# Kernel optimization log

Measured on AMD Instinct MI355X. Metric: run time of the kernel, lower is better.

The kernel has to match this reference:

```python
import jax, jax.numpy as jnp
import numpy as np

EPS = 1e-12  # F.normalize eps
G = 8        # groups (init g)
NC = 32      # num_cluster
LMD = 2


def _l2norm(v, axis):
    n = jnp.sqrt(jnp.sum(v * v, axis=axis, keepdims=True))
    return v / jnp.maximum(n, EPS)


def setup_inputs() -> dict:
    key = jax.random.key(0)
    ks = jax.random.split(key, 6)
    b, m, d = 32, 512, 1024
    d2 = LMD * d                 # 2048
    nd = d2 // G                 # 256 = new_dims
    x = jax.random.normal(ks[0], (b, m, d), dtype=jnp.float32)
    mask = jnp.ones((b, m), dtype=bool)
    # Linear params with torch-like fan-in scaling
    We = jax.random.normal(ks[1], (d2, d), dtype=jnp.float32) / np.sqrt(d)
    be = jnp.zeros((d2,), dtype=jnp.float32)
    W1 = jax.random.normal(ks[2], (G * NC, d2), dtype=jnp.float32) / np.sqrt(d2)
    b1 = jnp.zeros((G * NC,), dtype=jnp.float32)
    W2 = jax.random.normal(ks[3], (G, d2), dtype=jnp.float32) / np.sqrt(d2)
    b2 = jnp.zeros((G,), dtype=jnp.float32)
    centroid = jax.random.uniform(ks[4], (NC, nd), dtype=jnp.float32)
    return {"x": x, "mask": mask, "We": We, "be": be, "W1": W1, "b1": b1,
            "W2": W2, "b2": b2, "centroid": centroid}


def reference(x, mask, We, be, W1, b1, W2, b2, centroid):
    b, m, d = x.shape
    # BaseAggregator: L2 normalize along feature dim (mask unused)
    xn = _l2norm(x, axis=2)
    xe = jnp.einsum('bmd,ed->bme', xn, We) + be          # (b, m, lmd*d)
    a1 = jax.nn.softmax((jnp.einsum('bme,ke->bmk', xe, W1) + b1)
                        .reshape(b, m, G, NC), axis=3)   # (b, m, G, nc)
    a2 = jax.nn.softmax(jnp.einsum('bme,ge->bmg', xe, W2) + b2, axis=2)  # (b, m, G)
    xg = xe.reshape(b, m, G, -1)                         # (b, m, G, new_dims)
    # sum_nc a1*(x - c) = x*sum(a1) - a1@c = x - a1@c  (softmax sums to 1)
    cent = jnp.einsum('bmgk,kd->bmgd', a1, centroid)     # (b, m, G, new_dims)
    v = jnp.einsum('bmg,bmgd->bd', a2, xg - cent) / m    # sum over G, mean over m
    return _l2norm(v, axis=1)
```

## Files before the change

### kernel.cpp

```cpp
#include <hip/hip_runtime.h>
#include <hip/hip_bf16.h>
#include <stdint.h>

#define B_BATCH 32
#define M_SEQ   512
#define R_TOT   16384
#define D_IN    1024
#define E_DIM   2048
#define NCAT    384
#define NVALID  264

typedef float  f32x4 __attribute__((ext_vector_type(4)));
typedef short  s16x8 __attribute__((ext_vector_type(8)));

__device__ __forceinline__ uint16_t f2bf(float f) {
  uint32_t u = __builtin_bit_cast(uint32_t, f);
  uint32_t r = (u + 0x7fffu + ((u >> 16) & 1u)) >> 16;
  return (uint16_t)r;
}
__device__ __forceinline__ float bf2f(uint16_t u) {
  return __builtin_bit_cast(float, (uint32_t)u << 16);
}

__device__ __forceinline__ f32x4 mfma_bf16(s16x8 a, s16x8 b, f32x4 c) {
  return __builtin_amdgcn_mfma_f32_16x16x32_bf16(a, b, c, 0, 0, 0);
}

typedef __attribute__((address_space(3))) void lds_void_t;
typedef const __attribute__((address_space(1))) void gbl_void_t;
__device__ __forceinline__ void async_load16(const void* g, void* l) {
  __builtin_amdgcn_global_load_lds((gbl_void_t*)g, (lds_void_t*)l, 16, 0, 0);
}

#define FENCE() __builtin_amdgcn_sched_barrier(0)
#define PH_PRE_NL() do { FENCE(); __builtin_amdgcn_s_barrier(); FENCE(); \
                         __builtin_amdgcn_s_setprio(1); } while (0)
#define PH_POST() do { __builtin_amdgcn_s_setprio(0); FENCE(); \
                       __builtin_amdgcn_s_barrier(); FENCE(); } while (0)

__global__ void zero_buf(float* __restrict__ p, int n) {
  int i = blockIdx.x * blockDim.x + threadIdx.x;
  if (i < n) p[i] = 0.0f;
}

__global__ void cvt_bf16(const float* __restrict__ src, uint16_t* __restrict__ dst, int n) {
  int i = blockIdx.x * blockDim.x + threadIdx.x;
  if (i < n) dst[i] = f2bf(src[i]);
}

__global__ void build_wcat(const float* __restrict__ W1, const float* __restrict__ W2,
                           uint16_t* __restrict__ wcat) {
  int i = blockIdx.x * blockDim.x + threadIdx.x;
  if (i >= NCAT * E_DIM) return;
  int row = i >> 11, col = i & (E_DIM - 1);
  float v = 0.0f;
  if (row < 256) v = W1[i];
  else if (row < NVALID) v = W2[(row - 256) * E_DIM + col];
  wcat[i] = f2bf(v);
}

__global__ void build_bcat(const float* __restrict__ b1, const float* __restrict__ b2,
                           float* __restrict__ bcat) {
  int i = blockIdx.x * blockDim.x + threadIdx.x;
  if (i >= NCAT) return;
  float v = 0.0f;
  if (i < 256) v = b1[i];
  else if (i < NVALID) v = b2[i - 256];
  bcat[i] = v;
}

__global__ __launch_bounds__(256) void normalize_rows(const float* __restrict__ x,
                                                      uint16_t* __restrict__ xn) {
  const int r = blockIdx.x, tid = threadIdx.x;
  const float4* xr = (const float4*)(x + (size_t)r * D_IN);
  float4 v = xr[tid];
  float ss = v.x * v.x + v.y * v.y + v.z * v.z + v.w * v.w;
  #pragma unroll
  for (int m = 32; m; m >>= 1) ss += __shfl_xor(ss, m);
  __shared__ float wsum[4];
  if ((tid & 63) == 0) wsum[tid >> 6] = ss;
  __syncthreads();
  float tot = wsum[0] + wsum[1] + wsum[2] + wsum[3];
  float scale = 1.0f / fmaxf(sqrtf(tot), 1e-12f);
  uint16_t* o = xn + (size_t)r * D_IN + tid * 4;
  o[0] = f2bf(v.x * scale); o[1] = f2bf(v.y * scale);
  o[2] = f2bf(v.z * scale); o[3] = f2bf(v.w * scale);
}

template <int KDIM>
__global__ __launch_bounds__(512, 2) void gemm256(
    const uint16_t* __restrict__ A, const uint16_t* __restrict__ B,
    const float* __restrict__ bias, uint16_t* __restrict__ C, int N) {
  __shared__ uint16_t lds[65536];
  constexpr int NT = KDIM / 64;
  const int tid = threadIdx.x;
  const int w = tid >> 6, lane = tid & 63;
  const int wr = w >> 2, wc = w & 3;
  const int bm = blockIdx.x, bn = blockIdx.y;

  const int srow = tid >> 3;
  const int scol = (((tid & 7) ^ (srow & 7)) << 3);
  const int l15 = lane & 15, l4 = lane >> 4, lx = lane & 7;
  const int ck0 = ((l4) ^ lx) << 4;
  const int ck1 = ((4 + l4) ^ lx) << 4;

  const int arow0 = bm * 256, brow0 = bn * 256;

  auto STAGE = [&](const uint16_t* __restrict__ M, int grow0, int tile,
                   int bufi, int mat, int half) {
    if (tile >= NT) return;
    const uint16_t* src = M + (size_t)(grow0 + half * 128 + srow) * KDIM + tile * 64 + scol;
    uint16_t* dst = lds + ((bufi * 2 + mat) * 2 + half) * 8192 + w * 512;
    async_load16(src, dst);
    async_load16(src + (size_t)64 * KDIM, dst + 4096);
  };
  auto LDA = [&](int bufi, int mi, int ckb) -> s16x8 {
    return *(const s16x8*)((const char*)(lds + ((bufi * 2 + 0) * 2 + wr) * 8192)
                           + (mi * 16 + l15) * 128 + ckb);
  };
  auto LDB = [&](int bufi, int ni, int ckb) -> s16x8 {
    return *(const s16x8*)((const char*)(lds + ((bufi * 2 + 1) * 2 + (wc >> 1)) * 8192)
                           + ((wc & 1) * 64 + ni * 16 + l15) * 128 + ckb);
  };

  f32x4 acc[8][4] = {};
  s16x8 aLo[4][2], aHi[4][2], bLo[2][2], bHi[2][2];

  auto R1 = [&](int buf) {
    #pragma unroll
    for (int mi = 0; mi < 4; ++mi) { aLo[mi][0] = LDA(buf, mi, ck0); aLo[mi][1] = LDA(buf, mi, ck1); }
    #pragma unroll
    for (int ni = 0; ni < 2; ++ni) { bLo[ni][0] = LDB(buf, ni, ck0); bLo[ni][1] = LDB(buf, ni, ck1); }
  };
  auto R2 = [&](int buf) {
    #pragma unroll
    for (int j = 0; j < 2; ++j) { bHi[j][0] = LDB(buf, 2 + j, ck0); bHi[j][1] = LDB(buf, 2 + j, ck1); }
  };
  auto R3 = [&](int buf) {
    #pragma unroll
    for (int mi = 0; mi < 4; ++mi) { aHi[mi][0] = LDA(buf, 4 + mi, ck0); aHi[mi][1] = LDA(buf, 4 + mi, ck1); }
  };

  auto MM1 = [&] {
    #pragma unroll
    for (int kk = 0; kk < 2; ++kk)
      #pragma unroll
      for (int mi = 0; mi < 4; ++mi)
        #pragma unroll
        for (int ni = 0; ni < 2; ++ni)
          acc[mi][ni] = mfma_bf16(aLo[mi][kk], bLo[ni][kk], acc[mi][ni]);
  };
  auto MM2 = [&] {
    #pragma unroll
    for (int kk = 0; kk < 2; ++kk)
      #pragma unroll
      for (int mi = 0; mi < 4; ++mi)
        #pragma unroll
        for (int j = 0; j < 2; ++j)
          acc[mi][2 + j] = mfma_bf16(aLo[mi][kk], bHi[j][kk], acc[mi][2 + j]);
  };
  auto MM3 = [&] {
    #pragma unroll
    for (int kk = 0; kk < 2; ++kk)
      #pragma unroll
      for (int mi = 0; mi < 4; ++mi)
        #pragma unroll
        for (int ni = 0; ni < 2; ++ni)
          acc[4 + mi][ni] = mfma_bf16(aHi[mi][kk], bLo[ni][kk], acc[4 + mi][ni]);
  };
  auto MM4 = [&] {
    #pragma unroll
    for (int kk = 0; kk < 2; ++kk)
      #pragma unroll
      for (int mi = 0; mi < 4; ++mi)
        #pragma unroll
        for (int j = 0; j < 2; ++j)
          acc[4 + mi][2 + j] = mfma_bf16(aHi[mi][kk], bHi[j][kk], acc[4 + mi][2 + j]);
  };

#define GROUP(H, T, VM0, FINAL) do {                                           \
    STAGE(A, arow0, (T) + 1, (H) ^ 1, 0, 0);                                   \
    PH_PRE_NL(); R2(H); MM1(); PH_POST();                                      \
    STAGE(A, arow0, (T) + 1, (H) ^ 1, 0, 1);                                   \
    PH_PRE_NL(); R3(H); MM2(); PH_POST();                                      \
    STAGE(B, brow0, (T) + 2, (H), 1, 0);                                       \
    PH_PRE_NL(); MM3(); PH_POST();                                             \
    STAGE(B, brow0, (T) + 2, (H), 1, 1);                                       \
    FENCE();                                                                   \
    if (!(FINAL)) {                                                            \
      if (VM0) asm volatile("s_waitcnt vmcnt(0)" ::: "memory");                \
      else     asm volatile("s_waitcnt vmcnt(4)" ::: "memory");                \
    }                                                                          \
    __builtin_amdgcn_s_barrier(); FENCE();                                     \
    __builtin_amdgcn_s_setprio(1);                                             \
    if (!(FINAL)) R1((H) ^ 1);                                                 \
    MM4(); PH_POST();                                                          \
  } while (0)

  STAGE(A, arow0, 0, 0, 0, 0); STAGE(A, arow0, 0, 0, 0, 1);
  STAGE(B, brow0, 0, 0, 1, 0); STAGE(B, brow0, 0, 0, 1, 1);
  STAGE(B, brow0, 1, 1, 1, 0); STAGE(B, brow0, 1, 1, 1, 1);
  FENCE();
  asm volatile("s_waitcnt vmcnt(4)" ::: "memory");
  __builtin_amdgcn_s_barrier(); FENCE();
  R1(0);

  for (int i = 0; i < NT / 2 - 1; ++i) {
    GROUP(0, 2 * i, false, false);
    GROUP(1, 2 * i + 1, false, false);
  }
  GROUP(0, NT - 2, true, false);
  GROUP(1, NT - 1, false, true);
#undef GROUP

  asm volatile("s_nop 7\n\ts_nop 7\n\ts_nop 7" ::);

  const int lr0 = wr * 128 + l4 * 4;
  const int lc0 = wc * 64 + l15;
  #pragma unroll
  for (int ni = 0; ni < 4; ++ni) {
    const int col = lc0 + ni * 16;
    const float bv = bias[bn * 256 + col];
    const int c16 = col >> 3, c7 = col & 7;
    #pragma unroll
    for (int mi = 0; mi < 8; ++mi) {
      #pragma unroll
      for (int jj = 0; jj < 4; ++jj) {
        const int row = lr0 + mi * 16 + jj;
        lds[row * 256 + ((c16 ^ (row & 31)) << 3) + c7] = f2bf(acc[mi][ni][jj] + bv);
      }
    }
  }
  __syncthreads();
  {
    const int row = tid >> 1, ch = tid & 1;
    const int r31 = row & 31;
    uint16_t* dst = C + (size_t)(arow0 + row) * N + bn * 256 + ch * 128;
    #pragma unroll
    for (int q = 0; q < 8; ++q) {
      const int c16a = ch * 16 + 2 * q;
      s16x8 v0 = *(const s16x8*)&lds[row * 256 + ((c16a ^ r31) << 3)];
      s16x8 v1 = *(const s16x8*)&lds[row * 256 + (((c16a + 1) ^ r31) << 3)];
      *(s16x8*)(dst + q * 16) = v0;
      *(s16x8*)(dst + q * 16 + 8) = v1;
    }
  }
}

template <typename OutT>
__global__ __launch_bounds__(256, 2) void gemm_bt(
    const uint16_t* __restrict__ A, const uint16_t* __restrict__ B,
    const float* __restrict__ bias, OutT* __restrict__ C, int N, int K) {
  __shared__ __align__(16) uint16_t As[128 * 64];
  __shared__ __align__(16) uint16_t Bs[128 * 64];
  const int tid = threadIdx.x;
  const int w = tid >> 6, lane = tid & 63;
  const int wr = w >> 1, wc = w & 1;
  const int tm = blockIdx.x, tn = blockIdx.y;

  f32x4 acc[4][4] = {};

  const int lrow = lane >> 3;
  const int lk = (lane & 7) * 8;
  const size_t a_row0 = (size_t)tm * 128;
  const size_t b_row0 = (size_t)tn * 128;

  for (int k0 = 0; k0 < K; k0 += 64) {
    #pragma unroll
    for (int j = 0; j < 4; ++j) {
      const int c = w * 4 + j;
      const int row = c * 8 + lrow;
      async_load16(A + (a_row0 + row) * K + k0 + lk, (void*)(As + c * 512));
      async_load16(B + (b_row0 + row) * K + k0 + lk, (void*)(Bs + c * 512));
    }
    __syncthreads();
    #pragma unroll
    for (int kk = 0; kk < 2; ++kk) {
      const int krow = kk * 32 + (lane >> 4) * 8;
      s16x8 af[4], bfr[4];
      #pragma unroll
      for (int mi = 0; mi < 4; ++mi)
        af[mi] = *(const s16x8*)&As[(wr * 64 + mi * 16 + (lane & 15)) * 64 + krow];
      #pragma unroll
      for (int ni = 0; ni < 4; ++ni)
        bfr[ni] = *(const s16x8*)&Bs[(wc * 64 + ni * 16 + (lane & 15)) * 64 + krow];
      #pragma unroll
      for (int mi = 0; mi < 4; ++mi)
        #pragma unroll
        for (int ni = 0; ni < 4; ++ni)
          acc[mi][ni] = mfma_bf16(af[mi], bfr[ni], acc[mi][ni]);
    }
    __syncthreads();
  }
  asm volatile("s_nop 7\n\ts_nop 7\n\ts_nop 7" ::);

  const int rbase = wr * 64 + (lane >> 4) * 4;
  const int cbase = wc * 64 + (lane & 15);
  #pragma unroll
  for (int ni = 0; ni < 4; ++ni) {
    const int col = tn * 128 + cbase + ni * 16;
    const float bv = bias[col];
    #pragma unroll
    for (int mi = 0; mi < 4; ++mi) {
      #pragma unroll
      for (int jj = 0; jj < 4; ++jj) {
        const int row = tm * 128 + rbase + mi * 16 + jj;
        float v = acc[mi][ni][jj] + bv;
        if constexpr (sizeof(OutT) == 2) C[(size_t)row * N + col] = (OutT)f2bf(v);
        else                             C[(size_t)row * N + col] = v;
      }
    }
  }
}

__global__ __launch_bounds__(256) void softmax_accum(
    const float* __restrict__ logits,
    const uint16_t* __restrict__ xe,
    float* __restrict__ t1,
    float* __restrict__ sacc) {
  const int tid = threadIdx.x;
  const int r0 = blockIdx.x * 32;
  const int b = r0 >> 9;
  __shared__ float p1s[256];
  __shared__ float a2s[8];
  float t1_local = 0.0f, s_local = 0.0f;

  for (int rr = 0; rr < 32; ++rr) {
    const int r = r0 + rr;
    const float* lrow = logits + (size_t)r * NCAT;
    float lg = lrow[tid];
    float mx = lg;
    #pragma unroll
    for (int m = 16; m; m >>= 1) mx = fmaxf(mx, __shfl_xor(mx, m));
    float e = __expf(lg - mx);
    float sm = e;
    #pragma unroll
    for (int m = 16; m; m >>= 1) sm += __shfl_xor(sm, m);
    p1s[tid] = e / sm;
    if (tid < 8) {
      float l2 = lrow[256 + tid];
      float m2 = l2;
      #pragma unroll
      for (int m = 4; m; m >>= 1) m2 = fmaxf(m2, __shfl_xor(m2, m));
      float e2 = __expf(l2 - m2);
      float s2 = e2;
      #pragma unroll
      for (int m = 4; m; m >>= 1) s2 += __shfl_xor(s2, m);
      a2s[tid] = e2 / s2;
    }
    __syncthreads();
    const uint16_t* xr = xe + (size_t)r * E_DIM;
    float a = 0.0f;
    #pragma unroll
    for (int g = 0; g < 8; ++g) a += a2s[g] * bf2f(xr[g * 256 + tid]);
    t1_local += a;
    if (tid < 32) {
      float sa = 0.0f;
      #pragma unroll
      for (int g = 0; g < 8; ++g) sa += a2s[g] * p1s[g * 32 + tid];
      s_local += sa;
    }
    __syncthreads();
  }
  atomicAdd(&t1[b * 256 + tid], t1_local);
  if (tid < 32) atomicAdd(&sacc[b * 32 + tid], s_local);
}

__global__ __launch_bounds__(256) void finalize(const float* __restrict__ t1,
                                                const float* __restrict__ sacc,
                                                const float* __restrict__ centroid,
                                                float* __restrict__ out) {
  const int b = blockIdx.x, tid = threadIdx.x;
  float cs = 0.0f;
  #pragma unroll
  for (int k = 0; k < 32; ++k) cs += sacc[b * 32 + k] * centroid[k * 256 + tid];
  float v = (t1[b * 256 + tid] - cs) * (1.0f / (float)M_SEQ);
  float ss = v * v;
  #pragma unroll
  for (int m = 32; m; m >>= 1) ss += __shfl_xor(ss, m);
  __shared__ float wsum[4];
  if ((tid & 63) == 0) wsum[tid >> 6] = ss;
  __syncthreads();
  float tot = wsum[0] + wsum[1] + wsum[2] + wsum[3];
  out[b * 256 + tid] = v / fmaxf(sqrtf(tot), 1e-12f);
}

extern "C" void kernel_launch(void* const* d_in, const int* in_sizes, int n_in,
                              void* d_out, int out_size, void* d_ws, size_t ws_size,
                              hipStream_t stream) {
  const float* x        = (const float*)d_in[0];
  const float* We       = (const float*)d_in[2];
  const float* be       = (const float*)d_in[3];
  const float* W1       = (const float*)d_in[4];
  const float* b1       = (const float*)d_in[5];
  const float* W2       = (const float*)d_in[6];
  const float* b2       = (const float*)d_in[7];
  const float* centroid = (const float*)d_in[8];
  float* out = (float*)d_out;

  char* ws = (char*)d_ws;
  uint16_t* xe     = (uint16_t*)(ws + 0);
  uint16_t* xn     = (uint16_t*)(ws + 67108864);
  float*    logits = (float*)  (ws + 67108864);
  uint16_t* webf   = (uint16_t*)(ws + 100663296);
  uint16_t* wcat   = (uint16_t*)(ws + 104857600);
  float*    bcat   = (float*)  (ws + 106430464);
  float*    t1     = (float*)  (ws + 106432000);
  float*    sacc   = (float*)  (ws + 106464768);

  zero_buf  <<<dim3(36),   256, 0, stream>>>(t1, 8192 + 1024);
  cvt_bf16  <<<dim3(8192), 256, 0, stream>>>(We, webf, E_DIM * D_IN);
  build_wcat<<<dim3(3072), 256, 0, stream>>>(W1, W2, wcat);
  build_bcat<<<dim3(2),    256, 0, stream>>>(b1, b2, bcat);

  normalize_rows<<<dim3(R_TOT), 256, 0, stream>>>(x, xn);
  gemm256<D_IN><<<dim3(R_TOT / 256, E_DIM / 256), 512, 0, stream>>>(
      xn, webf, be, xe, E_DIM);
  gemm_bt<float><<<dim3(R_TOT / 128, NCAT / 128), 256, 0, stream>>>(
      xe, wcat, bcat, logits, NCAT, E_DIM);
  softmax_accum<<<dim3(R_TOT / 32), 256, 0, stream>>>(logits, xe, t1, sacc);
  finalize<<<dim3(B_BATCH), 256, 0, stream>>>(t1, sacc, centroid, out);
}
```

Measured before the change: 298.6 us.

## Drop sched barriers in GEMM pipeline and rewrite softmax_accum as barrier-free per-wave

Removes the compiler sched_barrier fences and trailing s_nop padding from the pipelined GEMM phases, so the compiler can schedule instructions across the phase boundaries. The softmax_accum kernel is restructured so each wave handles 8 rows on its own. It uses vectorized float4 and ushort4 loads and wave shuffles in place of shared memory and __syncthreads, and accumulates the centroid weights directly from the exponentials. The cost is more atomics per block. Removing the fences also risks the compiler reordering LDS reads or MFMAs across the carefully phased barriers.

Result: faster. 282.9 us (-5.3%).

```diff
diff --git a/kernel.cpp b/kernel.cpp
--- a/kernel.cpp
+++ b/kernel.cpp
@@ -32,11 +32,10 @@
   __builtin_amdgcn_global_load_lds((gbl_void_t*)g, (lds_void_t*)l, 16, 0, 0);
 }
 
-#define FENCE() __builtin_amdgcn_sched_barrier(0)
-#define PH_PRE_NL() do { FENCE(); __builtin_amdgcn_s_barrier(); FENCE(); \
-                         __builtin_amdgcn_s_setprio(1); } while (0)
-#define PH_POST() do { __builtin_amdgcn_s_setprio(0); FENCE(); \
-                       __builtin_amdgcn_s_barrier(); FENCE(); } while (0)
+#define PH_A() do { __builtin_amdgcn_s_barrier(); \
+                    __builtin_amdgcn_s_setprio(1); } while (0)
+#define PH_B() do { __builtin_amdgcn_s_setprio(0); \
+                    __builtin_amdgcn_s_barrier(); } while (0)
 
 __global__ void zero_buf(float* __restrict__ p, int n) {
   int i = blockIdx.x * blockDim.x + threadIdx.x;
@@ -180,29 +179,27 @@
 
 #define GROUP(H, T, VM0, FINAL) do {                                           \
     STAGE(A, arow0, (T) + 1, (H) ^ 1, 0, 0);                                   \
-    PH_PRE_NL(); R2(H); MM1(); PH_POST();                                      \
+    PH_A(); R2(H); MM1(); PH_B();                                              \
     STAGE(A, arow0, (T) + 1, (H) ^ 1, 0, 1);                                   \
-    PH_PRE_NL(); R3(H); MM2(); PH_POST();                                      \
+    PH_A(); R3(H); MM2(); PH_B();                                              \
     STAGE(B, brow0, (T) + 2, (H), 1, 0);                                       \
-    PH_PRE_NL(); MM3(); PH_POST();                                             \
+    PH_A(); MM3(); PH_B();                                                     \
     STAGE(B, brow0, (T) + 2, (H), 1, 1);                                       \
-    FENCE();                                                                   \
     if (!(FINAL)) {                                                            \
       if (VM0) asm volatile("s_waitcnt vmcnt(0)" ::: "memory");                \
       else     asm volatile("s_waitcnt vmcnt(4)" ::: "memory");                \
     }                                                                          \
-    __builtin_amdgcn_s_barrier(); FENCE();                                     \
+    __builtin_amdgcn_s_barrier();                                              \
     __builtin_amdgcn_s_setprio(1);                                             \
     if (!(FINAL)) R1((H) ^ 1);                                                 \
-    MM4(); PH_POST();                                                          \
+    MM4(); PH_B();                                                             \
   } while (0)
 
   STAGE(A, arow0, 0, 0, 0, 0); STAGE(A, arow0, 0, 0, 0, 1);
   STAGE(B, brow0, 0, 0, 1, 0); STAGE(B, brow0, 0, 0, 1, 1);
   STAGE(B, brow0, 1, 1, 1, 0); STAGE(B, brow0, 1, 1, 1, 1);
-  FENCE();
   asm volatile("s_waitcnt vmcnt(4)" ::: "memory");
-  __builtin_amdgcn_s_barrier(); FENCE();
+  __builtin_amdgcn_s_barrier();
   R1(0);
 
   for (int i = 0; i < NT / 2 - 1; ++i) {
@@ -212,8 +209,6 @@
   GROUP(0, NT - 2, true, false);
   GROUP(1, NT - 1, false, true);
 #undef GROUP
-
-  asm volatile("s_nop 7\n\ts_nop 7\n\ts_nop 7" ::);
 
   const int lr0 = wr * 128 + l4 * 4;
   const int lc0 = wc * 64 + l15;
@@ -292,7 +287,6 @@
     }
     __syncthreads();
   }
-  asm volatile("s_nop 7\n\ts_nop 7\n\ts_nop 7" ::);
 
   const int rbase = wr * 64 + (lane >> 4) * 4;
   const int cbase = wc * 64 + (lane & 15);
@@ -319,51 +313,64 @@
     float* __restrict__ t1,
     float* __restrict__ sacc) {
   const int tid = threadIdx.x;
-  const int r0 = blockIdx.x * 32;
-  const int b = r0 >> 9;
-  __shared__ float p1s[256];
-  __shared__ float a2s[8];
-  float t1_local = 0.0f, s_local = 0.0f;
-
-  for (int rr = 0; rr < 32; ++rr) {
+  const int lane = tid & 63, wv = tid >> 6;
+  const int r0 = blockIdx.x * 32 + wv * 8;
+  const int b = (blockIdx.x * 32) >> 9;
+  const int g = lane >> 3;
+  float t1v[4] = {0.f, 0.f, 0.f, 0.f};
+  float sv[4]  = {0.f, 0.f, 0.f, 0.f};
+
+  for (int rr = 0; rr < 8; ++rr) {
     const int r = r0 + rr;
     const float* lrow = logits + (size_t)r * NCAT;
-    float lg = lrow[tid];
-    float mx = lg;
-    #pragma unroll
-    for (int m = 16; m; m >>= 1) mx = fmaxf(mx, __shfl_xor(mx, m));
-    float e = __expf(lg - mx);
-    float sm = e;
-    #pragma unroll
-    for (int m = 16; m; m >>= 1) sm += __shfl_xor(sm, m);
-    p1s[tid] = e / sm;
-    if (tid < 8) {
-      float l2 = lrow[256 + tid];
-      float m2 = l2;
-      #pragma unroll
-      for (int m = 4; m; m >>= 1) m2 = fmaxf(m2, __shfl_xor(m2, m));
-      float e2 = __expf(l2 - m2);
-      float s2 = e2;
-      #pragma unroll
-      for (int m = 4; m; m >>= 1) s2 += __shfl_xor(s2, m);
-      a2s[tid] = e2 / s2;
-    }
-    __syncthreads();
-    const uint16_t* xr = xe + (size_t)r * E_DIM;
-    float a = 0.0f;
-    #pragma unroll
-    for (int g = 0; g < 8; ++g) a += a2s[g] * bf2f(xr[g * 256 + tid]);
-    t1_local += a;
-    if (tid < 32) {
-      float sa = 0.0f;
-      #pragma unroll
-      for (int g = 0; g < 8; ++g) sa += a2s[g] * p1s[g * 32 + tid];
-      s_local += sa;
-    }
-    __syncthreads();
-  }
-  atomicAdd(&t1[b * 256 + tid], t1_local);
-  if (tid < 32) atomicAdd(&sacc[b * 32 + tid], s_local);
+    float4 lg = *(const float4*)(lrow + 4 * lane);
+    float mx = fmaxf(fmaxf(lg.x, lg.y), fmaxf(lg.z, lg.w));
+    mx = fmaxf(mx, __shfl_xor(mx, 1));
+    mx = fmaxf(mx, __shfl_xor(mx, 2));
+    mx = fmaxf(mx, __shfl_xor(mx, 4));
+    float e0 = __expf(lg.x - mx), e1 = __expf(lg.y - mx);
+    float e2 = __expf(lg.z - mx), e3 = __expf(lg.w - mx);
+    float sm = e0 + e1 + e2 + e3;
+    sm += __shfl_xor(sm, 1); sm += __shfl_xor(sm, 2); sm += __shfl_xor(sm, 4);
+    const float inv = 1.0f / sm;
+    float4 la = *(const float4*)(lrow + 256);
+    float4 lb = *(const float4*)(lrow + 260);
+    float a2w[8] = {la.x, la.y, la.z, la.w, lb.x, lb.y, lb.z, lb.w};
+    float m2 = a2w[0];
+    #pragma unroll
+    for (int j = 1; j < 8; ++j) m2 = fmaxf(m2, a2w[j]);
+    float s2 = 0.0f;
+    #pragma unroll
+    for (int j = 0; j < 8; ++j) { a2w[j] = __expf(a2w[j] - m2); s2 += a2w[j]; }
+    const float i2 = 1.0f / s2;
+    #pragma unroll
+    for (int j = 0; j < 8; ++j) a2w[j] *= i2;
+    const uint16_t* xr = xe + (size_t)r * E_DIM + 4 * lane;
+    #pragma unroll
+    for (int gg = 0; gg < 8; ++gg) {
+      ushort4 xv = *(const ushort4*)(xr + gg * 256);
+      t1v[0] += a2w[gg] * bf2f(xv.x);
+      t1v[1] += a2w[gg] * bf2f(xv.y);
+      t1v[2] += a2w[gg] * bf2f(xv.z);
+      t1v[3] += a2w[gg] * bf2f(xv.w);
+    }
+    const float wgt = a2w[g] * inv;
+    sv[0] += wgt * e0; sv[1] += wgt * e1; sv[2] += wgt * e2; sv[3] += wgt * e3;
+  }
+  #pragma unroll
+  for (int e = 0; e < 4; ++e) {
+    sv[e] += __shfl_xor(sv[e], 8);
+    sv[e] += __shfl_xor(sv[e], 16);
+    sv[e] += __shfl_xor(sv[e], 32);
+  }
+  #pragma unroll
+  for (int e = 0; e < 4; ++e)
+    atomicAdd(&t1[b * 256 + 4 * lane + e], t1v[e]);
+  if (lane < 8) {
+    #pragma unroll
+    for (int e = 0; e < 4; ++e)
+      atomicAdd(&sacc[b * 32 + 4 * lane + e], sv[e]);
+  }
 }
 
 __global__ __launch_bounds__(256) void finalize(const float* __restrict__ t1,
```
